# Performance work log

Measured on AMD Instinct MI355X. Metric: run time of the kernel, lower is better.

The kernel has to match this reference:

```python
import jax, jax.numpy as jnp
import numpy as np

S = 128           # seq_len
B = 256           # input_bits (bits per token, also neurons per head)
H = 16            # num_heads
NB = 12           # n_bits_per_neuron -> LUT size 2^12
PB = 7            # relative-position bits = ceil(log2(max_seq_len))
HEAD_IN = 2 * B + PB   # concat(query, key, rel_pos_bits) = 519
THRESH = H // 2


def setup_inputs() -> dict:
    key = jax.random.key(0)
    k1, k2, k3 = jax.random.split(key, 3)
    tokens = jax.random.randint(k1, (S, B), 0, 2, dtype=jnp.int32)           # binary token bits
    memory = jax.random.normal(k2, (H, B, 2 ** NB), dtype=jnp.float32)       # RAM LUT contents per head/neuron
    connections = jax.random.randint(k3, (H, B, NB), 0, HEAD_IN, dtype=jnp.int32)  # per-neuron input-bit wiring
    return {"tokens": tokens, "memory": memory, "connections": connections}


def reference(tokens, memory, connections):
    idx = jnp.arange(S)
    rel = idx[:, None] - idx[None, :]                         # [S,S] i - j
    mask = (rel >= 0).astype(jnp.int32)                        # causal mask (j <= i)
    relc = jnp.clip(rel, 0, S - 1)
    # relative-distance binary encoding, LSB first: [S,S,PB]
    pos_bits = ((relc[..., None] >> jnp.arange(PB)) & 1).astype(jnp.int32)
    q = jnp.broadcast_to(tokens[:, None, :], (S, S, B))
    k = jnp.broadcast_to(tokens[None, :, :], (S, S, B))
    head_in = jnp.concatenate([q, k, pos_bits], axis=-1)       # [S,S,HEAD_IN]
    # RAM address per (query i, key j, head h, neuron n): pack NB wired bits, LSB first
    addr = jnp.zeros((S, S, H, B), dtype=jnp.int32)
    for b in range(NB):  # tiny fixed loop over bit planes, fully vectorized over S,S,H,B
        addr = addr + (head_in[..., connections[:, :, b]] << b)
    # LUT gather: memory[h, n, addr] -> [S,S,H,B]
    h_idx = jnp.arange(H)[:, None]
    n_idx = jnp.arange(B)[None, :]
    vals = memory[h_idx, n_idx, addr]
    bits = (vals > 0.0).astype(jnp.int32)                      # RAM neuron output bit
    # XOR accumulation over attended keys == masked sum mod 2: [S,H,B]
    head_res = jnp.sum(bits * mask[:, :, None, None], axis=1) % 2
    # majority vote across heads per bit
    ones_count = jnp.sum(head_res, axis=1)                     # [S,B]
    return (ones_count > THRESH).astype(jnp.int32)
```

## Files before the change

kernel.cpp:

```cpp
#include <hip/hip_runtime.h>
#include <hip/hip_bf16.h>


#define S 128
#define B 256
#define H 16
#define NB 12

typedef __attribute__((address_space(3))) void       lds_void;
typedef const __attribute__((address_space(1))) void glb_void;

__device__ __forceinline__ void async16(const float* g, float* l) {
    __builtin_amdgcn_global_load_lds((glb_void*)g, (lds_void*)l, 16, 0, 0);
}

__global__ __launch_bounds__(1024) void softram_kernel(
    const int* __restrict__ tokens,
    const float* __restrict__ memory,
    const int* __restrict__ connections,
    int* __restrict__ out)
{
    const int n    = blockIdx.x;
    const int tid  = threadIdx.x;
    const int wv   = tid >> 6;
    const int lane = tid & 63;

    __shared__ float          raw[2][8192];
    __shared__ unsigned char  lutb[8192];
    __shared__ unsigned int   tok[S * 8];
    __shared__ unsigned short aks[H][S];
    __shared__ unsigned short aps[H][S];
    __shared__ unsigned short aqs[H][S];
    __shared__ int            conns[H][NB];
    __shared__ unsigned char  parts_r[2][S][8];
    __shared__ unsigned char  parts_all[S][H];

    auto issue_round = [&](int r, int buf) {
        #pragma unroll
        for (int q = 0; q < 2; ++q) {
            int c = wv * 2 + q;
            int h = 2 * r + (c >> 4);
            const float* g = memory + ((size_t)(h * 256 + n) << 12)
                           + ((c & 15) << 8) + (lane << 2);
            float* l = &raw[buf][c << 8];
            async16(g, l);
        }
    };

    auto pack_round = [&](int buf) {
        const float4* rp = (const float4*)&raw[buf][0];
        float4 a = rp[2 * tid], b4 = rp[2 * tid + 1];
        unsigned w0 = (unsigned)(a.x > 0.f)        | ((unsigned)(a.y > 0.f) << 8)
                    | ((unsigned)(a.z > 0.f) << 16)| ((unsigned)(a.w > 0.f) << 24);
        unsigned w1 = (unsigned)(b4.x > 0.f)       | ((unsigned)(b4.y > 0.f) << 8)
                    | ((unsigned)(b4.z > 0.f) << 16)|((unsigned)(b4.w > 0.f) << 24);
        ((uint2*)lutb)[tid] = make_uint2(w0, w1);
    };

    issue_round(0, 0);
    {
        int i = tid >> 3, w = tid & 7;
        const int4* tp = (const int4*)tokens;
        unsigned int t = 0;
        #pragma unroll
        for (int u = 0; u < 8; ++u) {
            int4 x = tp[i * 64 + w * 8 + u];
            t |= (unsigned)(x.x & 1) << (4 * u + 0);
            t |= (unsigned)(x.y & 1) << (4 * u + 1);
            t |= (unsigned)(x.z & 1) << (4 * u + 2);
            t |= (unsigned)(x.w & 1) << (4 * u + 3);
        }
        tok[tid] = t;
    }
    if (tid < H * NB) {
        int h = tid / NB, b = tid - h * NB;
        conns[h][b] = connections[h * (B * NB) + n * NB + b];
    }
    __syncthreads();

    issue_round(1, 1);

    #pragma unroll
    for (int e0 = 0; e0 < 2; ++e0) {
        int e = tid + (e0 << 10);
        int h = e >> 7, ii = e & 127;
        unsigned aq = 0, ak = 0, ap = 0;
        #pragma unroll
        for (int b = 0; b < NB; ++b) {
            int c = conns[h][b];
            if (c < 256) {
                aq |= ((tok[ii * 8 + (c >> 5)] >> (c & 31)) & 1u) << b;
            } else if (c < 512) {
                int c2 = c - 256;
                ak |= ((tok[ii * 8 + (c2 >> 5)] >> (c2 & 31)) & 1u) << b;
            } else {
                ap |= (unsigned)((ii >> (c - 512)) & 1) << b;
            }
        }
        aqs[h][ii] = (unsigned short)aq;
        aks[h][ii] = (unsigned short)ak;
        aps[h][ii] = (unsigned short)ap;
    }
    pack_round(0);
    __syncthreads();

    const int hh  = wv >> 3;
    const int res = wv & 7;
    const int i0 = lane, i1 = 127 - lane;
    const int c0 = (i0 >= res) ? (((i0 - res) >> 3) + 1) : 0;
    const int ct = c0 + (((i1 - res) >> 3) + 1);
    const unsigned char* __restrict__ lrow = &lutb[hh << 12];

    for (int r = 0; r < 8; ++r) {
        if (r < 6) issue_round(r + 2, r & 1);

        const int h = 2 * r + hh;
        const unsigned aq0 = aqs[h][i0], aq1 = aqs[h][i1];
        const unsigned short* __restrict__ akr = &aks[h][0];
        const unsigned short* __restrict__ apr = &aps[h][0];
        unsigned accA = 0, accB = 0;
        #pragma unroll
        for (int k = 0; k < 17; ++k) {
            bool first = (k < c0);
            int j   = res + ((first ? k : (k - c0)) << 3);
            int ii  = first ? i0 : i1;
            int imj = (ii - j) & 127;
            j &= 127;
            unsigned addr = (first ? aq0 : aq1) | akr[j] | apr[imj];
            unsigned v  = lrow[addr & 4095];
            unsigned vv = (k < ct) ? v : 0u;
            accA ^= first ? vv : 0u;
            accB ^= first ? 0u : vv;
        }
        parts_r[hh][i0][res] = (unsigned char)(accA & 1u);
        parts_r[hh][i1][res] = (unsigned char)(accB & 1u);

        __syncthreads();

        if (tid < 2 * S) {
            int ph = tid >> 7, i = tid & 127;
            uint2 pw = ((const uint2*)&parts_r[ph][i][0])[0];
            unsigned x = pw.x ^ pw.y;
            x ^= x >> 16; x ^= x >> 8;
            parts_all[i][2 * r + ph] = (unsigned char)(x & 1u);
        }
        if (r < 7) pack_round((r + 1) & 1);

        __syncthreads();
    }

    if (tid < S) {
        const unsigned char* pa = &parts_all[tid][0];
        int tot = 0;
        #pragma unroll
        for (int h2 = 0; h2 < H; ++h2) tot += pa[h2];
        out[tid * B + n] = (tot > (H / 2)) ? 1 : 0;
    }
}

extern "C" void kernel_launch(void* const* d_in, const int* in_sizes, int n_in,
                              void* d_out, int out_size, void* d_ws, size_t ws_size,
                              hipStream_t stream) {
    const int*   tokens      = (const int*)d_in[0];
    const float* memory      = (const float*)d_in[1];
    const int*   connections = (const int*)d_in[2];
    int*         out         = (int*)d_out;
    (void)in_sizes; (void)n_in; (void)out_size; (void)d_ws; (void)ws_size;

    softram_kernel<<<B, 1024, 0, stream>>>(tokens, memory, connections, out);
}
```

Baseline: 114.3 us.

## Use wave ballot/popcount parity on float LUT directly, drop byte-LUT packing

Removes the per-round byte-LUT packing pass and the cross-wave partial-parity reduction. Each wave now looks up the float LUT straight from the async-loaded staging buffer, one query per ballot with lanes covering keys. The causal XOR parity is formed with __ballot plus a masked popcount. The position-bit lookup is skipped for heads with no position wiring, and one barrier per round is dropped. In exchange it evaluates masked-out key positions too, and prefetches only one round ahead, so more load latency may be exposed at the barrier.

```diff
diff --git a/kernel.cpp b/kernel.cpp
--- a/kernel.cpp
+++ b/kernel.cpp
@@ -25,36 +25,25 @@
     const int wv   = tid >> 6;
     const int lane = tid & 63;
 
-    __shared__ float          raw[2][8192];
-    __shared__ unsigned char  lutb[8192];
+    __shared__ float          raw[2][2][4096];
     __shared__ unsigned int   tok[S * 8];
+    __shared__ unsigned short aqs[H][S];
     __shared__ unsigned short aks[H][S];
     __shared__ unsigned short aps[H][S];
-    __shared__ unsigned short aqs[H][S];
     __shared__ int            conns[H][NB];
-    __shared__ unsigned char  parts_r[2][S][8];
-    __shared__ unsigned char  parts_all[S][H];
+    __shared__ int            hasP[H];
+    __shared__ unsigned char  partsA[H][8];
+    __shared__ unsigned char  partsB[H][8];
 
     auto issue_round = [&](int r, int buf) {
         #pragma unroll
-        for (int q = 0; q < 2; ++q) {
-            int c = wv * 2 + q;
-            int h = 2 * r + (c >> 4);
-            const float* g = memory + ((size_t)(h * 256 + n) << 12)
+        for (int q2 = 0; q2 < 2; ++q2) {
+            int c = wv * 2 + q2;
+            const float* g = memory + ((size_t)((2 * r + (c >> 4)) * 256 + n) << 12)
                            + ((c & 15) << 8) + (lane << 2);
-            float* l = &raw[buf][c << 8];
+            float* l = &raw[buf][c >> 4][(c & 15) << 8];
             async16(g, l);
         }
-    };
-
-    auto pack_round = [&](int buf) {
-        const float4* rp = (const float4*)&raw[buf][0];
-        float4 a = rp[2 * tid], b4 = rp[2 * tid + 1];
-        unsigned w0 = (unsigned)(a.x > 0.f)        | ((unsigned)(a.y > 0.f) << 8)
-                    | ((unsigned)(a.z > 0.f) << 16)| ((unsigned)(a.w > 0.f) << 24);
-        unsigned w1 = (unsigned)(b4.x > 0.f)       | ((unsigned)(b4.y > 0.f) << 8)
-                    | ((unsigned)(b4.z > 0.f) << 16)|((unsigned)(b4.w > 0.f) << 24);
-        ((uint2*)lutb)[tid] = make_uint2(w0, w1);
     };
 
     issue_round(0, 0);
@@ -80,6 +69,12 @@
 
     issue_round(1, 1);
 
+    if (tid < H) {
+        int f = 0;
+        #pragma unroll
+        for (int b = 0; b < NB; ++b) f |= (conns[tid][b] >= 512);
+        hasP[tid] = f;
+    }
     #pragma unroll
     for (int e0 = 0; e0 < 2; ++e0) {
         int e = tid + (e0 << 10);
@@ -101,60 +96,68 @@
         aks[h][ii] = (unsigned short)ak;
         aps[h][ii] = (unsigned short)ap;
     }
-    pack_round(0);
     __syncthreads();
 
-    const int hh  = wv >> 3;
-    const int res = wv & 7;
-    const int i0 = lane, i1 = 127 - lane;
-    const int c0 = (i0 >= res) ? (((i0 - res) >> 3) + 1) : 0;
-    const int ct = c0 + (((i1 - res) >> 3) + 1);
-    const unsigned char* __restrict__ lrow = &lutb[hh << 12];
-
+    const int hh = wv & 1;
+    const int q  = wv >> 1;
     for (int r = 0; r < 8; ++r) {
-        if (r < 6) issue_round(r + 2, r & 1);
+        if (r < 7) issue_round(r + 1, (r + 1) & 1);
 
         const int h = 2 * r + hh;
-        const unsigned aq0 = aqs[h][i0], aq1 = aqs[h][i1];
-        const unsigned short* __restrict__ akr = &aks[h][0];
-        const unsigned short* __restrict__ apr = &aps[h][0];
+        const float* __restrict__ lrow = &raw[r & 1][hh][0];
+        const unsigned ak0 = aks[h][lane];
+        const unsigned ak1 = aks[h][lane + 64];
+        const bool hp = (hasP[h] != 0);
         unsigned accA = 0, accB = 0;
-        #pragma unroll
-        for (int k = 0; k < 17; ++k) {
-            bool first = (k < c0);
-            int j   = res + ((first ? k : (k - c0)) << 3);
-            int ii  = first ? i0 : i1;
-            int imj = (ii - j) & 127;
-            j &= 127;
-            unsigned addr = (first ? aq0 : aq1) | akr[j] | apr[imj];
-            unsigned v  = lrow[addr & 4095];
-            unsigned vv = (k < ct) ? v : 0u;
-            accA ^= first ? vv : 0u;
-            accB ^= first ? 0u : vv;
+
+        {
+            uint4 aqw = *(const uint4*)&aqs[h][q * 8];
+            const unsigned short* aqp = (const unsigned short*)&aqw;
+            #pragma unroll
+            for (int t = 0; t < 8; ++t) {
+                int i = q * 8 + t;
+                unsigned ap0 = hp ? (unsigned)aps[h][(i - lane) & 127] : 0u;
+                float v0 = lrow[aqp[t] + ak0 + ap0];
+                unsigned long long m0 = __ballot(v0 > 0.0f);
+                unsigned long long c0 = (2ull << i) - 1;
+                accA |= (unsigned)(__popcll(m0 & c0) & 1) << t;
+            }
         }
-        parts_r[hh][i0][res] = (unsigned char)(accA & 1u);
-        parts_r[hh][i1][res] = (unsigned char)(accB & 1u);
-
-        __syncthreads();
-
-        if (tid < 2 * S) {
-            int ph = tid >> 7, i = tid & 127;
-            uint2 pw = ((const uint2*)&parts_r[ph][i][0])[0];
-            unsigned x = pw.x ^ pw.y;
-            x ^= x >> 16; x ^= x >> 8;
-            parts_all[i][2 * r + ph] = (unsigned char)(x & 1u);
+        {
+            uint4 aqw = *(const uint4*)&aqs[h][64 + q * 8];
+            const unsigned short* aqp = (const unsigned short*)&aqw;
+            #pragma unroll
+            for (int t = 0; t < 8; ++t) {
+                int i = 64 + q * 8 + t;
+                unsigned ap0 = 0, ap1 = 0;
+                if (hp) {
+                    ap0 = aps[h][(i - lane) & 127];
+                    ap1 = aps[h][(i - lane - 64) & 127];
+                }
+                float v0 = lrow[aqp[t] + ak0 + ap0];
+                float v1 = lrow[aqp[t] + ak1 + ap1];
+                unsigned long long m0 = __ballot(v0 > 0.0f);
+                unsigned long long m1 = __ballot(v1 > 0.0f);
+                unsigned long long c1 = (2ull << (i - 64)) - 1;
+                accB |= (unsigned)((__popcll(m0) + __popcll(m1 & c1)) & 1) << t;
+            }
         }
-        if (r < 7) pack_round((r + 1) & 1);
-
+        if (lane == 0) {
+            partsA[h][q] = (unsigned char)accA;
+            partsB[h][q] = (unsigned char)accB;
+        }
         __syncthreads();
     }
 
     if (tid < S) {
-        const unsigned char* pa = &parts_all[tid][0];
+        int i = tid;
         int tot = 0;
         #pragma unroll
-        for (int h2 = 0; h2 < H; ++h2) tot += pa[h2];
-        out[tid * B + n] = (tot > (H / 2)) ? 1 : 0;
+        for (int h2 = 0; h2 < H; ++h2) {
+            unsigned bits = (i < 64) ? partsA[h2][i >> 3] : partsB[h2][(i - 64) >> 3];
+            tot += (bits >> (i & 7)) & 1;
+        }
+        out[i * B + n] = (tot > (H / 2)) ? 1 : 0;
     }
 }
 
```

Measured after the change: 126.2 us. +10.4%, slower.
